# Kernel tuning notes

Hardware: AMD Instinct MI355X
Metric: run time of the kernel (lower is better)

Reference implementation:

```python
import jax, jax.numpy as jnp
import numpy as np

N_HEAD = 16
NEG_BIG = 1e10

def setup_inputs() -> dict:
    key = jax.random.key(0)
    k1, k2, k3 = jax.random.split(key, 3)
    B, S, D = 2, 2048, 1024
    x = jax.random.normal(k1, (B, S, D), dtype=jnp.float32)
    c_attn_w = jax.random.normal(k2, (D, 3 * D), dtype=jnp.float32) * 0.02
    c_attn_b = jnp.zeros((3 * D,), dtype=jnp.float32)
    c_proj_w = jax.random.normal(k3, (D, D), dtype=jnp.float32) * 0.02
    c_proj_b = jnp.zeros((D,), dtype=jnp.float32)
    return {"x": x, "c_attn_w": c_attn_w, "c_attn_b": c_attn_b,
            "c_proj_w": c_proj_w, "c_proj_b": c_proj_b}

def reference(x, c_attn_w, c_attn_b, c_proj_w, c_proj_b):
    B, S, D = x.shape
    H = N_HEAD
    hd = D // H
    # Conv1D c_attn: x @ W + b -> (B, S, 3D)
    qkv = x @ c_attn_w + c_attn_b
    q, k, v = jnp.split(qkv, 3, axis=-1)
    # split heads -> (B, H, S, hd)
    q = q.reshape(B, S, H, hd).transpose(0, 2, 1, 3)
    k = k.reshape(B, S, H, hd).transpose(0, 2, 1, 3)
    v = v.reshape(B, S, H, hd).transpose(0, 2, 1, 3)
    # QK^T with scale (scale=True)
    w = jnp.einsum('bhqd,bhkd->bhqk', q, k) / jnp.sqrt(jnp.float32(hd))
    # additive/multiplicative causal mask, exactly as source: w*b - 1e10*(1-b)
    b = jnp.tril(jnp.ones((S, S), dtype=w.dtype))
    w = w * b - NEG_BIG * (1.0 - b)
    w = jax.nn.softmax(w, axis=-1)
    a = jnp.einsum('bhqk,bhkd->bhqd', w, v)
    # merge heads -> (B, S, D)
    a = a.transpose(0, 2, 1, 3).reshape(B, S, D)
    # Conv1D c_proj
    a = a @ c_proj_w + c_proj_b
    # present = stack(key (as (B,H,S,hd)), value)
    present = jnp.stack((k, v))
    return (a, present)
```

## Files before the change

kernel.cpp:

```cpp
#include <hip/hip_runtime.h>
#include <hip/hip_bf16.h>
#include <string.h>

#define BB 2
#define SS 2048
#define DD 1024
#define NH 16
#define TT (BB * SS)
#define N3 (3 * DD)
#define A_SIZE (TT * DD)
#define PRESENT_HALF (BB * NH * SS * 64)
#define C2Q 0.18033688011112043f

typedef __attribute__((ext_vector_type(8))) short short8;
typedef __attribute__((ext_vector_type(4))) float floatx4;
typedef __attribute__((ext_vector_type(8))) unsigned short ushort8;

__device__ __forceinline__ unsigned short f2bf(float f) {
    union { float f; unsigned u; } v; v.f = f;
    unsigned r = v.u + 0x7fffu + ((v.u >> 16) & 1u);
    return (unsigned short)(r >> 16);
}
__device__ __forceinline__ unsigned pack2bf(float a, float b) {
    __hip_bfloat162 h = __float22bfloat162_rn(float2{a, b});
    unsigned u; memcpy(&u, &h, 4); return u;
}
__device__ __forceinline__ float bf2f(unsigned short u) {
    union { unsigned u; float f; } v; v.u = ((unsigned)u) << 16; return v.f;
}

__device__ __forceinline__ void async16(const unsigned short* g, unsigned short* lds) {
    __builtin_amdgcn_global_load_lds(
        (const __attribute__((address_space(1))) unsigned int*)g,
        (__attribute__((address_space(3))) unsigned int*)lds,
        16, 0, 0);
}

__global__ __launch_bounds__(256) void cast_x_kernel(const float* __restrict__ src,
                                                     unsigned short* __restrict__ dst) {
    int i = (blockIdx.x * 256 + threadIdx.x) * 8;
    float4 a = *(const float4*)(src + i);
    float4 b = *(const float4*)(src + i + 4);
    ushort8 o;
    o[0] = f2bf(a.x); o[1] = f2bf(a.y); o[2] = f2bf(a.z); o[3] = f2bf(a.w);
    o[4] = f2bf(b.x); o[5] = f2bf(b.y); o[6] = f2bf(b.z); o[7] = f2bf(b.w);
    *(ushort8*)(dst + i) = o;
}

__global__ __launch_bounds__(256) void transpose_cast_kernel(const float* __restrict__ src,
                                                             unsigned short* __restrict__ dst,
                                                             int R, int C) {
    __shared__ float tile[32][33];
    int c0 = blockIdx.x * 32, r0 = blockIdx.y * 32;
    int tx = threadIdx.x, ty = threadIdx.y;
    for (int i = ty; i < 32; i += 8)
        tile[i][tx] = src[(size_t)(r0 + i) * C + c0 + tx];
    __syncthreads();
    for (int i = ty; i < 32; i += 8)
        dst[(size_t)(c0 + i) * R + r0 + tx] = f2bf(tile[tx][i]);
}

__global__ __launch_bounds__(256)
void vtrans_kernel(const unsigned short* __restrict__ qkv,
                   unsigned short* __restrict__ vT) {
    __shared__ unsigned short tile[64][72];
    int bh = blockIdx.x, st = blockIdx.y;
    int b = bh >> 4, h = bh & 15;
    int tid = threadIdx.x;
    int r = tid >> 2, c = (tid & 3) * 16;
    const unsigned short* src = qkv + ((size_t)(b * SS + st * 64 + r)) * 3072 + 2048 + h * 64 + c;
    *(int4*)(&tile[r][c])     = *(const int4*)(src);
    *(int4*)(&tile[r][c + 8]) = *(const int4*)(src + 8);
    __syncthreads();
    int d = tid >> 2, s0 = (tid & 3) * 16;
    unsigned short tmp[16];
    for (int e = 0; e < 16; ++e) tmp[e] = tile[s0 + e][d];
    unsigned short* dst = vT + ((size_t)bh * 64 + d) * SS + st * 64 + s0;
    *(int4*)(dst)     = *(const int4*)(tmp);
    *(int4*)(dst + 8) = *(const int4*)(tmp + 8);
}

__global__ __launch_bounds__(256)
void present_kernel(const unsigned short* __restrict__ qkvb, float* __restrict__ out) {
    size_t e = ((size_t)blockIdx.x * 256 + threadIdx.x) * 8;
    int d = (int)(e & 63);
    int s = (int)((e >> 6) & 2047);
    int h = (int)((e >> 17) & 15);
    int b = (int)((e >> 21) & 1);
    int half = (int)(e >> 22);
    const unsigned short* src = qkvb + ((size_t)(b * SS + s)) * 3072 + 1024 + half * 1024 + h * 64 + d;
    ushort8 u = *(const ushort8*)src;
    float* dst = out + A_SIZE + e;
    float4 f0 = {bf2f(u[0]), bf2f(u[1]), bf2f(u[2]), bf2f(u[3])};
    float4 f1 = {bf2f(u[4]), bf2f(u[5]), bf2f(u[6]), bf2f(u[7])};
    *(float4*)(dst) = f0;
    *(float4*)(dst + 4) = f1;
}

__global__ __launch_bounds__(256)
void gemm_kernel(const unsigned short* __restrict__ A,
                 const unsigned short* __restrict__ Bt,
                 const float* __restrict__ bias,
                 int mode,
                 unsigned short* __restrict__ out_bf,
                 float* __restrict__ out_f) {
    __shared__ unsigned short As[2][128][32];
    __shared__ unsigned short Bs[2][128][32];
    const int tid  = threadIdx.x;
    const int t0   = blockIdx.y * 128;
    const int n0   = blockIdx.x * 128;
    const int wave = tid >> 6, lane = tid & 63;
    const int wm = wave >> 1, wn = wave & 1;
    const int l15 = lane & 15, quad = lane >> 4;

    const int sr = lane >> 2;
    const int sc = (lane & 3) * 8;

    floatx4 acc[4][4];
    for (int i = 0; i < 4; ++i)
        for (int j = 0; j < 4; ++j)
            for (int e = 0; e < 4; ++e) acc[i][j][e] = 0.f;

    const unsigned short* gA = A  + (size_t)(t0 + wave * 32 + sr) * 1024 + sc;
    const unsigned short* gB = Bt + (size_t)(n0 + wave * 32 + sr) * 1024 + sc;

    async16(gA,             &As[0][wave * 32][0]);
    async16(gA + 16 * 1024, &As[0][wave * 32 + 16][0]);
    async16(gB,             &Bs[0][wave * 32][0]);
    async16(gB + 16 * 1024, &Bs[0][wave * 32 + 16][0]);

    for (int kt = 0; kt < 32; ++kt) {
        const int cur = kt & 1;
        __syncthreads();
        if (kt < 31) {
            const int k1 = (kt + 1) * 32;
            async16(gA + k1,             &As[cur ^ 1][wave * 32][0]);
            async16(gA + k1 + 16 * 1024, &As[cur ^ 1][wave * 32 + 16][0]);
            async16(gB + k1,             &Bs[cur ^ 1][wave * 32][0]);
            async16(gB + k1 + 16 * 1024, &Bs[cur ^ 1][wave * 32 + 16][0]);
        }
        short8 af[4], bfr[4];
        for (int mt = 0; mt < 4; ++mt)
            af[mt] = *(const short8*)(&As[cur][wm * 64 + mt * 16 + l15][quad * 8]);
        for (int nt = 0; nt < 4; ++nt)
            bfr[nt] = *(const short8*)(&Bs[cur][wn * 64 + nt * 16 + l15][quad * 8]);
        for (int mt = 0; mt < 4; ++mt)
            for (int nt = 0; nt < 4; ++nt)
                acc[mt][nt] = __builtin_amdgcn_mfma_f32_16x16x32_bf16(bfr[nt], af[mt], acc[mt][nt], 0, 0, 0);
    }

    const float qs = (mode == 0 && n0 < 1024) ? C2Q : 1.0f;
    for (int mt = 0; mt < 4; ++mt) {
        const int t = t0 + wm * 64 + mt * 16 + l15;
        if (mode == 0) {
            unsigned short* po = out_bf + (size_t)t * 3072 + n0 + wn * 64;
            for (int nt = 0; nt < 4; ++nt) {
                float4 b4 = *(const float4*)(bias + n0 + wn * 64 + nt * 16 + quad * 4);
                float v0 = (acc[mt][nt][0] + b4.x) * qs;
                float v1 = (acc[mt][nt][1] + b4.y) * qs;
                float v2 = (acc[mt][nt][2] + b4.z) * qs;
                float v3 = (acc[mt][nt][3] + b4.w) * qs;
                uint2 w = {pack2bf(v0, v1), pack2bf(v2, v3)};
                *(uint2*)(po + nt * 16 + quad * 4) = w;
            }
        } else {
            float* po = out_f + (size_t)t * 1024 + n0 + wn * 64;
            for (int nt = 0; nt < 4; ++nt) {
                float4 b4 = *(const float4*)(bias + n0 + wn * 64 + nt * 16 + quad * 4);
                float4 v = {acc[mt][nt][0] + b4.x, acc[mt][nt][1] + b4.y,
                            acc[mt][nt][2] + b4.z, acc[mt][nt][3] + b4.w};
                *(float4*)(po + nt * 16 + quad * 4) = v;
            }
        }
    }
}

__global__ __launch_bounds__(256)
void flash_kernel(const unsigned short* __restrict__ qkv,
                  const unsigned short* __restrict__ vT,
                  unsigned short* __restrict__ out) {
    __shared__ unsigned short Kt[2][64][72];
    __shared__ unsigned short Vt[2][64][72];
    __shared__ unsigned short Pt[4][16][72];

    const int bh = blockIdx.x;
    const int qt = 31 - blockIdx.y;
    const int b = bh >> 4, h = bh & 15;
    const int tid = threadIdx.x;
    const int wave = tid >> 6, lane = tid & 63;
    const int l15 = lane & 15, quad = lane >> 4;

    const size_t rowb = (size_t)b * SS;
    const int kcol = 1024 + h * 64;

    short8 bq0, bq1;
    {
        const unsigned short* qp = qkv + (rowb + qt * 64 + wave * 16 + l15) * 3072 + h * 64 + quad * 8;
        bq0 = *(const short8*)(qp);
        bq1 = *(const short8*)(qp + 32);
    }

    float l_i = 0.f;
    floatx4 o[4];
    for (int dt = 0; dt < 4; ++dt)
        for (int e = 0; e < 4; ++e) o[dt][e] = 0.f;

    const int qrow_l = wave * 16 + l15;

    const int rr = tid >> 3, seg = (tid & 7) * 8;
    const int vr = tid >> 2, vc = (tid & 3) * 16;
    const unsigned short* kb = qkv + rowb * 3072 + kcol;
    const unsigned short* vb = vT + (size_t)bh * 64 * SS;
    int4 ka0, ka1, va0, va1;

    #define PREF(j) { \
        const unsigned short* ks = kb + (size_t)((j) * 64 + rr) * 3072 + seg; \
        ka0 = *(const int4*)(ks); \
        ka1 = *(const int4*)(ks + 32 * 3072); \
        const unsigned short* vs = vb + (size_t)vr * SS + (j) * 64 + vc; \
        va0 = *(const int4*)(vs); \
        va1 = *(const int4*)(vs + 8); }
    #define STAGE(bf_) { \
        *(int4*)(&Kt[bf_][rr][seg])      = ka0; \
        *(int4*)(&Kt[bf_][rr + 32][seg]) = ka1; \
        *(int4*)(&Vt[bf_][vr][vc])       = va0; \
        *(int4*)(&Vt[bf_][vr][vc + 8])   = va1; }

    PREF(0);
    STAGE(0);
    if (qt > 0) PREF(1);

    for (int j = 0; j <= qt; ++j) {
        const int cur = j & 1;
        __syncthreads();
        if (j < qt) {
            STAGE(cur ^ 1);
            if (j + 2 <= qt) PREF(j + 2);
        }

        floatx4 sc[4];
        for (int nt = 0; nt < 4; ++nt)
            for (int e = 0; e < 4; ++e) sc[nt][e] = 0.f;
        for (int nt = 0; nt < 4; ++nt) {
            const unsigned short* kp = &Kt[cur][nt * 16 + l15][quad * 8];
            short8 ak0 = *(const short8*)(kp);
            short8 ak1 = *(const short8*)(kp + 32);
            sc[nt] = __builtin_amdgcn_mfma_f32_16x16x32_bf16(ak0, bq0, sc[nt], 0, 0, 0);
            sc[nt] = __builtin_amdgcn_mfma_f32_16x16x32_bf16(ak1, bq1, sc[nt], 0, 0, 0);
        }
        if (j == qt) {
            for (int nt = 0; nt < 4; ++nt)
                for (int r = 0; r < 4; ++r)
                    if (nt * 16 + quad * 4 + r > qrow_l) sc[nt][r] = -1.0e30f;
        }

        for (int nt = 0; nt < 4; ++nt)
            for (int r = 0; r < 4; ++r) {
                float p = __builtin_amdgcn_exp2f(sc[nt][r]);
                sc[nt][r] = p;
                l_i += p;
            }

        for (int nt = 0; nt < 4; ++nt) {
            uint2 w = {pack2bf(sc[nt][0], sc[nt][1]), pack2bf(sc[nt][2], sc[nt][3])};
            *(uint2*)(&Pt[wave][l15][nt * 16 + quad * 4]) = w;
        }
        asm volatile("s_waitcnt lgkmcnt(0)" ::: "memory");
        short8 bp0 = *(const short8*)(&Pt[wave][l15][quad * 8]);
        short8 bp1 = *(const short8*)(&Pt[wave][l15][32 + quad * 8]);
        for (int dt = 0; dt < 4; ++dt) {
            const unsigned short* vp = &Vt[cur][dt * 16 + l15][quad * 8];
            short8 av0 = *(const short8*)(vp);
            short8 av1 = *(const short8*)(vp + 32);
            o[dt] = __builtin_amdgcn_mfma_f32_16x16x32_bf16(av0, bp0, o[dt], 0, 0, 0);
            o[dt] = __builtin_amdgcn_mfma_f32_16x16x32_bf16(av1, bp1, o[dt], 0, 0, 0);
        }
    }
    #undef PREF
    #undef STAGE

    l_i += __shfl_xor(l_i, 16);
    l_i += __shfl_xor(l_i, 32);
    float inv = 1.f / l_i;
    const int qrow = qt * 64 + wave * 16 + l15;
    unsigned short* po = out + (rowb + qrow) * 1024 + h * 64;
    for (int dt = 0; dt < 4; ++dt) {
        uint2 w = {pack2bf(o[dt][0] * inv, o[dt][1] * inv),
                   pack2bf(o[dt][2] * inv, o[dt][3] * inv)};
        *(uint2*)(po + dt * 16 + quad * 4) = w;
    }
}

extern "C" void kernel_launch(void* const* d_in, const int* in_sizes, int n_in,
                              void* d_out, int out_size, void* d_ws, size_t ws_size,
                              hipStream_t stream) {
    const float* x        = (const float*)d_in[0];
    const float* c_attn_w = (const float*)d_in[1];
    const float* c_attn_b = (const float*)d_in[2];
    const float* c_proj_w = (const float*)d_in[3];
    const float* c_proj_b = (const float*)d_in[4];
    float* out = (float*)d_out;

    char* ws = (char*)d_ws;
    unsigned short* xb     = (unsigned short*)(ws);
    unsigned short* wqkvt  = (unsigned short*)(ws + 8388608);
    unsigned short* wprojt = (unsigned short*)(ws + 14680064);
    unsigned short* qkvb   = (unsigned short*)(ws + 16777216);
    unsigned short* aout   = (unsigned short*)(ws + 41943040);
    unsigned short* vT     = xb;

    cast_x_kernel<<<(TT * DD) / (256 * 8), 256, 0, stream>>>(x, xb);
    transpose_cast_kernel<<<dim3(N3 / 32, DD / 32), dim3(32, 8), 0, stream>>>(c_attn_w, wqkvt, DD, N3);
    transpose_cast_kernel<<<dim3(DD / 32, DD / 32), dim3(32, 8), 0, stream>>>(c_proj_w, wprojt, DD, DD);
    gemm_kernel<<<dim3(N3 / 128, TT / 128), 256, 0, stream>>>(xb, wqkvt, c_attn_b, 0, qkvb, out);
    present_kernel<<<(2 * PRESENT_HALF) / (256 * 8), 256, 0, stream>>>(qkvb, out);
    vtrans_kernel<<<dim3(32, 32), 256, 0, stream>>>(qkvb, vT);
    flash_kernel<<<dim3(32, 32), 256, 0, stream>>>(qkvb, vT, aout);
    gemm_kernel<<<dim3(DD / 128, TT / 128), 256, 0, stream>>>(aout, wprojt, c_proj_b, 1, nullptr, out);
}
```

Baseline: 215.5 us.

## Triple-buffer GEMM with fragment-ordered LDS, fuse present write into V transpose, add setprio

The GEMM moves from a double-buffered to a triple-buffered async LDS pipeline. Tiles are stored in MFMA-fragment order so each lane reads contiguously, with explicit vmcnt waits and one barrier per k-step, plus s_setprio around the MFMA blocks and launch bounds for 3 blocks per CU. The separate present kernel is merged into the V-transpose kernel, so K/V are read once to produce both vT and the fp32 present output, saving a launch and a pass over qkv. Flash attention also gets s_setprio around its MFMA loops. The risks are the hand-placed waitcnt and barrier logic and higher LDS use per block.

```diff
diff --git a/kernel.cpp b/kernel.cpp
--- a/kernel.cpp
+++ b/kernel.cpp
@@ -11,6 +11,7 @@
 #define A_SIZE (TT * DD)
 #define PRESENT_HALF (BB * NH * SS * 64)
 #define C2Q 0.18033688011112043f
+#define NKT 32
 
 typedef __attribute__((ext_vector_type(8))) short short8;
 typedef __attribute__((ext_vector_type(4))) float floatx4;
@@ -61,18 +62,39 @@
 }
 
 __global__ __launch_bounds__(256)
-void vtrans_kernel(const unsigned short* __restrict__ qkv,
-                   unsigned short* __restrict__ vT) {
+void pv_kernel(const unsigned short* __restrict__ qkv,
+               unsigned short* __restrict__ vT,
+               float* __restrict__ out) {
     __shared__ unsigned short tile[64][72];
-    int bh = blockIdx.x, st = blockIdx.y;
-    int b = bh >> 4, h = bh & 15;
-    int tid = threadIdx.x;
-    int r = tid >> 2, c = (tid & 3) * 16;
-    const unsigned short* src = qkv + ((size_t)(b * SS + st * 64 + r)) * 3072 + 2048 + h * 64 + c;
-    *(int4*)(&tile[r][c])     = *(const int4*)(src);
-    *(int4*)(&tile[r][c + 8]) = *(const int4*)(src + 8);
+    const int bh = blockIdx.x, st = blockIdx.y;
+    const int b = bh >> 4, h = bh & 15;
+    const int tid = threadIdx.x;
+    const int r = tid >> 2, c = (tid & 3) * 16;
+    const size_t row = (size_t)(b * SS + st * 64 + r);
+
+    const unsigned short* srcv = qkv + row * 3072 + 2048 + h * 64 + c;
+    ushort8 v0 = *(const ushort8*)(srcv);
+    ushort8 v1 = *(const ushort8*)(srcv + 8);
+    *(ushort8*)(&tile[r][c])     = v0;
+    *(ushort8*)(&tile[r][c + 8]) = v1;
+    float* dv = out + A_SIZE + PRESENT_HALF + ((size_t)bh * SS + st * 64 + r) * 64 + c;
+    float4 f;
+    f = {bf2f(v0[0]), bf2f(v0[1]), bf2f(v0[2]), bf2f(v0[3])}; *(float4*)(dv)      = f;
+    f = {bf2f(v0[4]), bf2f(v0[5]), bf2f(v0[6]), bf2f(v0[7])}; *(float4*)(dv + 4)  = f;
+    f = {bf2f(v1[0]), bf2f(v1[1]), bf2f(v1[2]), bf2f(v1[3])}; *(float4*)(dv + 8)  = f;
+    f = {bf2f(v1[4]), bf2f(v1[5]), bf2f(v1[6]), bf2f(v1[7])}; *(float4*)(dv + 12) = f;
+
+    const unsigned short* srck = qkv + row * 3072 + 1024 + h * 64 + c;
+    ushort8 k0 = *(const ushort8*)(srck);
+    ushort8 k1 = *(const ushort8*)(srck + 8);
+    float* dk = out + A_SIZE + ((size_t)bh * SS + st * 64 + r) * 64 + c;
+    f = {bf2f(k0[0]), bf2f(k0[1]), bf2f(k0[2]), bf2f(k0[3])}; *(float4*)(dk)      = f;
+    f = {bf2f(k0[4]), bf2f(k0[5]), bf2f(k0[6]), bf2f(k0[7])}; *(float4*)(dk + 4)  = f;
+    f = {bf2f(k1[0]), bf2f(k1[1]), bf2f(k1[2]), bf2f(k1[3])}; *(float4*)(dk + 8)  = f;
+    f = {bf2f(k1[4]), bf2f(k1[5]), bf2f(k1[6]), bf2f(k1[7])}; *(float4*)(dk + 12) = f;
+
     __syncthreads();
-    int d = tid >> 2, s0 = (tid & 3) * 16;
+    const int d = tid >> 2, s0 = (tid & 3) * 16;
     unsigned short tmp[16];
     for (int e = 0; e < 16; ++e) tmp[e] = tile[s0 + e][d];
     unsigned short* dst = vT + ((size_t)bh * 64 + d) * SS + st * 64 + s0;
@@ -80,80 +102,84 @@
     *(int4*)(dst + 8) = *(const int4*)(tmp + 8);
 }
 
-__global__ __launch_bounds__(256)
-void present_kernel(const unsigned short* __restrict__ qkvb, float* __restrict__ out) {
-    size_t e = ((size_t)blockIdx.x * 256 + threadIdx.x) * 8;
-    int d = (int)(e & 63);
-    int s = (int)((e >> 6) & 2047);
-    int h = (int)((e >> 17) & 15);
-    int b = (int)((e >> 21) & 1);
-    int half = (int)(e >> 22);
-    const unsigned short* src = qkvb + ((size_t)(b * SS + s)) * 3072 + 1024 + half * 1024 + h * 64 + d;
-    ushort8 u = *(const ushort8*)src;
-    float* dst = out + A_SIZE + e;
-    float4 f0 = {bf2f(u[0]), bf2f(u[1]), bf2f(u[2]), bf2f(u[3])};
-    float4 f1 = {bf2f(u[4]), bf2f(u[5]), bf2f(u[6]), bf2f(u[7])};
-    *(float4*)(dst) = f0;
-    *(float4*)(dst + 4) = f1;
-}
-
-__global__ __launch_bounds__(256)
+__global__ __launch_bounds__(256, 3)
 void gemm_kernel(const unsigned short* __restrict__ A,
                  const unsigned short* __restrict__ Bt,
                  const float* __restrict__ bias,
                  int mode,
                  unsigned short* __restrict__ out_bf,
                  float* __restrict__ out_f) {
-    __shared__ unsigned short As[2][128][32];
-    __shared__ unsigned short Bs[2][128][32];
-    const int tid  = threadIdx.x;
-    const int t0   = blockIdx.y * 128;
-    const int n0   = blockIdx.x * 128;
+    __shared__ unsigned short As3[3][8][512];
+    __shared__ unsigned short Bs3[3][8][512];
+    const int tid = threadIdx.x;
     const int wave = tid >> 6, lane = tid & 63;
+    const int l15 = lane & 15, quad = lane >> 4;
     const int wm = wave >> 1, wn = wave & 1;
-    const int l15 = lane & 15, quad = lane >> 4;
-
-    const int sr = lane >> 2;
-    const int sc = (lane & 3) * 8;
+    const int t0 = blockIdx.y * 128;
+    const int n0 = blockIdx.x * 128;
 
     floatx4 acc[4][4];
+    #pragma unroll
     for (int i = 0; i < 4; ++i)
+        #pragma unroll
         for (int j = 0; j < 4; ++j)
+            #pragma unroll
             for (int e = 0; e < 4; ++e) acc[i][j][e] = 0.f;
 
-    const unsigned short* gA = A  + (size_t)(t0 + wave * 32 + sr) * 1024 + sc;
-    const unsigned short* gB = Bt + (size_t)(n0 + wave * 32 + sr) * 1024 + sc;
-
-    async16(gA,             &As[0][wave * 32][0]);
-    async16(gA + 16 * 1024, &As[0][wave * 32 + 16][0]);
-    async16(gB,             &Bs[0][wave * 32][0]);
-    async16(gB + 16 * 1024, &Bs[0][wave * 32 + 16][0]);
-
-    for (int kt = 0; kt < 32; ++kt) {
-        const int cur = kt & 1;
-        __syncthreads();
-        if (kt < 31) {
-            const int k1 = (kt + 1) * 32;
-            async16(gA + k1,             &As[cur ^ 1][wave * 32][0]);
-            async16(gA + k1 + 16 * 1024, &As[cur ^ 1][wave * 32 + 16][0]);
-            async16(gB + k1,             &Bs[cur ^ 1][wave * 32][0]);
-            async16(gB + k1 + 16 * 1024, &Bs[cur ^ 1][wave * 32 + 16][0]);
-        }
+    const unsigned short* gA = A  + (size_t)(t0 + wave * 32 + l15) * 1024 + quad * 8;
+    const unsigned short* gB = Bt + (size_t)(n0 + wave * 32 + l15) * 1024 + quad * 8;
+
+    #define STAGE(buf_, koff_) {                                        \
+        async16(gA + (koff_),             &As3[buf_][wave * 2][0]);     \
+        async16(gA + (koff_) + 16 * 1024, &As3[buf_][wave * 2 + 1][0]); \
+        async16(gB + (koff_),             &Bs3[buf_][wave * 2][0]);     \
+        async16(gB + (koff_) + 16 * 1024, &Bs3[buf_][wave * 2 + 1][0]); }
+
+    STAGE(0, 0);
+    STAGE(1, 32);
+    asm volatile("s_waitcnt vmcnt(4)" ::: "memory");
+    __builtin_amdgcn_s_barrier();
+    asm volatile("" ::: "memory");
+
+    int cur = 0, nx2 = 2;
+    for (int t = 0; t < NKT; ++t) {
+        if (t < NKT - 2) STAGE(nx2, (t + 2) * 32);
+
+        const unsigned short* aB = &As3[cur][wm * 4][0] + lane * 8;
+        const unsigned short* bB = &Bs3[cur][wn * 4][0] + lane * 8;
         short8 af[4], bfr[4];
+        #pragma unroll
+        for (int mt = 0; mt < 4; ++mt) af[mt]  = *(const short8*)(aB + mt * 512);
+        #pragma unroll
+        for (int nt = 0; nt < 4; ++nt) bfr[nt] = *(const short8*)(bB + nt * 512);
+
+        __builtin_amdgcn_s_setprio(1);
+        #pragma unroll
         for (int mt = 0; mt < 4; ++mt)
-            af[mt] = *(const short8*)(&As[cur][wm * 64 + mt * 16 + l15][quad * 8]);
-        for (int nt = 0; nt < 4; ++nt)
-            bfr[nt] = *(const short8*)(&Bs[cur][wn * 64 + nt * 16 + l15][quad * 8]);
-        for (int mt = 0; mt < 4; ++mt)
+            #pragma unroll
             for (int nt = 0; nt < 4; ++nt)
                 acc[mt][nt] = __builtin_amdgcn_mfma_f32_16x16x32_bf16(bfr[nt], af[mt], acc[mt][nt], 0, 0, 0);
-    }
+        __builtin_amdgcn_s_setprio(0);
+
+        asm volatile("s_waitcnt lgkmcnt(0)" ::: "memory");
+        if (t < NKT - 2) { asm volatile("s_waitcnt vmcnt(4)" ::: "memory"); }
+        else             { asm volatile("s_waitcnt vmcnt(0)" ::: "memory"); }
+        asm volatile("" ::: "memory");
+        __builtin_amdgcn_s_barrier();
+        asm volatile("" ::: "memory");
+
+        cur = (cur == 2) ? 0 : cur + 1;
+        nx2 = (nx2 == 2) ? 0 : nx2 + 1;
+    }
+    #undef STAGE
 
     const float qs = (mode == 0 && n0 < 1024) ? C2Q : 1.0f;
+    #pragma unroll
     for (int mt = 0; mt < 4; ++mt) {
         const int t = t0 + wm * 64 + mt * 16 + l15;
         if (mode == 0) {
             unsigned short* po = out_bf + (size_t)t * 3072 + n0 + wn * 64;
+            #pragma unroll
             for (int nt = 0; nt < 4; ++nt) {
                 float4 b4 = *(const float4*)(bias + n0 + wn * 64 + nt * 16 + quad * 4);
                 float v0 = (acc[mt][nt][0] + b4.x) * qs;
@@ -165,6 +191,7 @@
             }
         } else {
             float* po = out_f + (size_t)t * 1024 + n0 + wn * 64;
+            #pragma unroll
             for (int nt = 0; nt < 4; ++nt) {
                 float4 b4 = *(const float4*)(bias + n0 + wn * 64 + nt * 16 + quad * 4);
                 float4 v = {acc[mt][nt][0] + b4.x, acc[mt][nt][1] + b4.y,
@@ -241,6 +268,7 @@
         floatx4 sc[4];
         for (int nt = 0; nt < 4; ++nt)
             for (int e = 0; e < 4; ++e) sc[nt][e] = 0.f;
+        __builtin_amdgcn_s_setprio(1);
         for (int nt = 0; nt < 4; ++nt) {
             const unsigned short* kp = &Kt[cur][nt * 16 + l15][quad * 8];
             short8 ak0 = *(const short8*)(kp);
@@ -248,6 +276,7 @@
             sc[nt] = __builtin_amdgcn_mfma_f32_16x16x32_bf16(ak0, bq0, sc[nt], 0, 0, 0);
             sc[nt] = __builtin_amdgcn_mfma_f32_16x16x32_bf16(ak1, bq1, sc[nt], 0, 0, 0);
         }
+        __builtin_amdgcn_s_setprio(0);
         if (j == qt) {
             for (int nt = 0; nt < 4; ++nt)
                 for (int r = 0; r < 4; ++r)
@@ -268,6 +297,7 @@
         asm volatile("s_waitcnt lgkmcnt(0)" ::: "memory");
         short8 bp0 = *(const short8*)(&Pt[wave][l15][quad * 8]);
         short8 bp1 = *(const short8*)(&Pt[wave][l15][32 + quad * 8]);
+        __builtin_amdgcn_s_setprio(1);
         for (int dt = 0; dt < 4; ++dt) {
             const unsigned short* vp = &Vt[cur][dt * 16 + l15][quad * 8];
             short8 av0 = *(const short8*)(vp);
@@ -275,6 +305,7 @@
             o[dt] = __builtin_amdgcn_mfma_f32_16x16x32_bf16(av0, bp0, o[dt], 0, 0, 0);
             o[dt] = __builtin_amdgcn_mfma_f32_16x16x32_bf16(av1, bp1, o[dt], 0, 0, 0);
         }
+        __builtin_amdgcn_s_setprio(0);
     }
     #undef PREF
     #undef STAGE
@@ -312,9 +343,8 @@
     cast_x_kernel<<<(TT * DD) / (256 * 8), 256, 0, stream>>>(x, xb);
     transpose_cast_kernel<<<dim3(N3 / 32, DD / 32), dim3(32, 8), 0, stream>>>(c_attn_w, wqkvt, DD, N3);
     transpose_cast_kernel<<<dim3(DD / 32, DD / 32), dim3(32, 8), 0, stream>>>(c_proj_w, wprojt, DD, DD);
-    gemm_kernel<<<dim3(N3 / 128, TT / 128), 256, 0, stream>>>(xb, wqkvt, c_attn_b, 0, qkvb, out);
-    present_kernel<<<(2 * PRESENT_HALF) / (256 * 8), 256, 0, stream>>>(qkvb, out);
-    vtrans_kernel<<<dim3(32, 32), 256, 0, stream>>>(qkvb, vT);
+    gemm_kernel<<<dim3(N3 / 128, TT / 128), 256, 0, stream>>>(xb, wqkvt, c_attn_b, 0, qkvb, nullptr);
+    pv_kernel<<<dim3(32, 32), 256, 0, stream>>>(qkvb, vT, out);
     flash_kernel<<<dim3(32, 32), 256, 0, stream>>>(qkvb, vT, aout);
     gemm_kernel<<<dim3(DD / 128, TT / 128), 256, 0, stream>>>(aout, wprojt, c_proj_b, 1, nullptr, out);
 }
```

New measurement: 240.3 us. 1.12x slower.
